# Optimization experiments

Measured on AMD Instinct MI355X. Metric: run time of the kernel, lower is better.

Reference implementation:

```python
import jax, jax.numpy as jnp
import numpy as np

B, S, D, H = 2, 2048, 2048, 16
HD = D // H  # head_dim = 128


def rotate_half(x):
    x1, x2 = x[..., : x.shape[-1] // 2], x[..., x.shape[-1] // 2 :]
    return jnp.concatenate((-x2, x1), axis=-1)


def setup_inputs() -> dict:
    key = jax.random.key(0)
    ks = jax.random.split(key, 6)
    x = jax.random.normal(ks[0], (B, S, D), dtype=jnp.float32)
    # RoPE cos/sin tables, shape [B, S, head_dim]
    inv_freq = 1.0 / (10000.0 ** (np.arange(0, HD, 2, dtype=np.float32) / HD))
    t = np.arange(S, dtype=np.float32)
    freqs = np.outer(t, inv_freq)                      # [S, HD/2]
    emb = np.concatenate([freqs, freqs], axis=-1)      # [S, HD]
    cos = jnp.broadcast_to(jnp.cos(emb), (B, S, HD)).astype(jnp.float32)
    sin = jnp.broadcast_to(jnp.sin(emb), (B, S, HD)).astype(jnp.float32)
    attn_mask = jnp.zeros((B, S), dtype=jnp.float32)   # additive 2D mask
    scale = 0.02
    wq = jax.random.normal(ks[1], (D, D), dtype=jnp.float32) * scale
    wk = jax.random.normal(ks[2], (D, D), dtype=jnp.float32) * scale
    wv = jax.random.normal(ks[3], (D, D), dtype=jnp.float32) * scale
    wo = jax.random.normal(ks[4], (D, D), dtype=jnp.float32) * scale
    return {"x": x, "cos": cos, "sin": sin, "attn_mask": attn_mask,
            "wq": wq, "wk": wk, "wv": wv, "wo": wo}


def reference(x, cos, sin, attn_mask, wq, wk, wv, wo):
    b, s, d = x.shape
    # fused-style QKV projections (nn.Linear: y = x @ W.T), reshape to [b,h,s,hd]
    def proj(w):
        return jnp.einsum('bsd,ed->bse', x, w).reshape(b, s, H, HD).transpose(0, 2, 1, 3)
    q, k, v = proj(wq), proj(wk), proj(wv)
    # RoPE: cos/sin [b,s,hd] -> broadcast over heads
    c = cos[:, None, :, :]
    sn = sin[:, None, :, :]
    q = q * c + rotate_half(q) * sn
    k = k * c + rotate_half(k) * sn
    # SDPA with additive 2D mask -> [b,1,1,s]
    scores = jnp.einsum('bhqd,bhkd->bhqk', q, k) / jnp.sqrt(jnp.float32(HD))
    scores = scores + attn_mask[:, None, None, :]
    attn = jax.nn.softmax(scores, axis=-1)
    out = jnp.einsum('bhqk,bhkd->bhqd', attn, v)
    out = out.transpose(0, 2, 1, 3).reshape(b, s, d)
    return jnp.einsum('bsd,ed->bse', out, wo)
```

## Files before the change

### kernel.cpp

```cpp
#include <hip/hip_runtime.h>

#define B_  2
#define S_  2048
#define D_  2048
#define H_  16
#define HD_ 128

typedef float  f32x4  __attribute__((ext_vector_type(4)));
typedef float  f32x16 __attribute__((ext_vector_type(16)));
typedef __bf16 bf16x8 __attribute__((ext_vector_type(8)));
typedef unsigned int u32;

__device__ __forceinline__ void gl16(const void* g, void* l) {
  __builtin_amdgcn_global_load_lds(
      (const __attribute__((address_space(1))) unsigned int*)g,
      (__attribute__((address_space(3))) unsigned int*)l, 16, 0, 0);
}

__device__ __forceinline__ ushort f2bf(float f) {
  union { float f; unsigned u; } v; v.f = f;
  unsigned r = v.u + 0x7FFFu + ((v.u >> 16) & 1u);
  return (ushort)(r >> 16);
}
__device__ __forceinline__ float bf2f(ushort b) {
  union { unsigned u; float f; } v; v.u = ((unsigned)b) << 16;
  return v.f;
}
__device__ __forceinline__ f32x4 fzero() {
  f32x4 v; v[0] = 0.f; v[1] = 0.f; v[2] = 0.f; v[3] = 0.f; return v;
}
__device__ __forceinline__ float exp2x(float x) {
  return __builtin_amdgcn_exp2f(x);
}

__global__ void cvt_all(const float* __restrict__ x,  const float* __restrict__ wq,
                        const float* __restrict__ wk, const float* __restrict__ wv,
                        const float* __restrict__ wo, ushort* __restrict__ dst)
{
  int i = blockIdx.x * blockDim.x + threadIdx.x;
  if (i >= 6291456) return;
  const float* s;
  int t = i - 2097152;
  if (t < 0)             { s = x;  t = i; }
  else if (t < 1048576)  { s = wq; }
  else if (t < 2097152)  { s = wk; t -= 1048576; }
  else if (t < 3145728)  { s = wv; t -= 2097152; }
  else                   { s = wo; t -= 3145728; }
  float4 v = ((const float4*)s)[t];
  ((ushort4*)dst)[i] = make_ushort4(f2bf(v.x), f2bf(v.y), f2bf(v.z), f2bf(v.w));
}

template<int MODE>
__global__ __launch_bounds__(256, 2)
void gemm_bt(const ushort* __restrict__ A, const ushort* __restrict__ Bp,
             void* __restrict__ Cp, int M, int N, int K)
{
  __shared__ __align__(16) ushort lds[2][2][128 * 32];
  const int tid  = threadIdx.x;
  const int wave = tid >> 6, lane = tid & 63;
  const int qt = lane >> 4, ln = lane & 15;
  const int wr = wave >> 1, wc = wave & 1;
  const int bm = blockIdx.x * 128, bn = blockIdx.y * 128;

  f32x4 acc[4][4];
#pragma unroll
  for (int a = 0; a < 4; ++a)
#pragma unroll
    for (int b = 0; b < 4; ++b) acc[a][b] = fzero();

  auto stage = [&](int buf, int kt) {
#pragma unroll
    for (int it = 0; it < 2; ++it) {
      int c = it * 256 + tid;
      int row = c >> 2, ch = c & 3;
      int chs = ch ^ ((row >> 1) & 3);
      gl16(A  + (size_t)(bm + row) * K + kt + chs * 8,
           (void*)&lds[buf][0][(it * 256 + wave * 64) * 8]);
      gl16(Bp + (size_t)(bn + row) * K + kt + chs * 8,
           (void*)&lds[buf][1][(it * 256 + wave * 64) * 8]);
    }
  };

  const int nk = K >> 5;
  stage(0, 0);
  int cur = 0;
  for (int kt = 0; kt < nk; ++kt) {
    __syncthreads();
    if (kt + 1 < nk) stage(cur ^ 1, (kt + 1) << 5);
    bf16x8 af[4], bfr[4];
#pragma unroll
    for (int mf = 0; mf < 4; ++mf) {
      int row = wr * 64 + mf * 16 + ln;
      int sl = qt ^ ((row >> 1) & 3);
      af[mf] = *(const bf16x8*)&lds[cur][0][row * 32 + sl * 8];
    }
#pragma unroll
    for (int nf = 0; nf < 4; ++nf) {
      int row = wc * 64 + nf * 16 + ln;
      int sl = qt ^ ((row >> 1) & 3);
      bfr[nf] = *(const bf16x8*)&lds[cur][1][row * 32 + sl * 8];
    }
#pragma unroll
    for (int mf = 0; mf < 4; ++mf)
#pragma unroll
      for (int nf = 0; nf < 4; ++nf)
        acc[mf][nf] = __builtin_amdgcn_mfma_f32_16x16x32_bf16(
            af[mf], bfr[nf], acc[mf][nf], 0, 0, 0);
    cur ^= 1;
  }

#pragma unroll
  for (int mf = 0; mf < 4; ++mf)
#pragma unroll
    for (int nf = 0; nf < 4; ++nf) {
      int m0 = bm + wr * 64 + mf * 16 + qt * 4;
      int n  = bn + wc * 64 + nf * 16 + ln;
#pragma unroll
      for (int i = 0; i < 4; ++i) {
        int m = m0 + i;
        if (MODE == 0) {
          ((float*)Cp)[(size_t)m * N + n] = acc[mf][nf][i];
        } else {
          int b = m >> 11, s = m & 2047;
          int h = n >> 7,  d = n & 127;
          if (MODE == 1)
            ((ushort*)Cp)[(((size_t)b * H_ + h) * S_ + s) * HD_ + d] = f2bf(acc[mf][nf][i]);
          else
            ((ushort*)Cp)[(((size_t)b * H_ + h) * HD_ + d) * S_ + s] = f2bf(acc[mf][nf][i]);
        }
      }
    }
}

__global__ void rope_qk(ushort* __restrict__ Q, ushort* __restrict__ Kt,
                        const float* __restrict__ cs, const float* __restrict__ sn)
{
  int t = blockIdx.x * 256 + threadIdx.x;
  int d  = t & 63;
  int rr = t >> 6;
  int isk = rr >> 16;
  int bhs = rr & 65535;
  int s = bhs & 2047;
  int b = bhs >> 15;
  ushort* P = isk ? Kt : Q;
  size_t ro = (size_t)bhs * HD_;
  float q0 = bf2f(P[ro + d]), q1 = bf2f(P[ro + d + 64]);
  size_t ci = ((size_t)b * S_ + s) * HD_ + d;
  float c0 = cs[ci], s0 = sn[ci], c1 = cs[ci + 64], s1 = sn[ci + 64];
  P[ro + d]      = f2bf(q0 * c0 - q1 * s0);
  P[ro + d + 64] = f2bf(q1 * c1 + q0 * s1);
}

__global__ __launch_bounds__(256, 2)
void flash(const ushort* __restrict__ Q, const ushort* __restrict__ Kk,
           const ushort* __restrict__ VT, const float* __restrict__ mask,
           ushort* __restrict__ O)
{
  __shared__ __align__(16) ushort kt_s[2][64 * 128];
  __shared__ __align__(16) ushort vt_s[2][128 * 64];

  const int tid = threadIdx.x;
  const int wave = tid >> 6, lane = tid & 63;
  const int ln32 = lane & 31, hi = lane >> 5;
  const int bh = blockIdx.x, b = bh >> 4, h = bh & 15;
  const size_t base  = (size_t)bh * S_ * HD_;
  const size_t baseT = (size_t)bh * HD_ * S_;
  const int q0 = blockIdx.y * 128 + wave * 32;
  const float L2E = 1.4426950408889634f;
  const float scale2 = 0.08838834764831845f * L2E;

  bf16x8 qf[8];
  {
    const ushort* qrow = Q + base + (size_t)(q0 + ln32) * HD_;
#pragma unroll
    for (int hd = 0; hd < 8; ++hd)
      qf[hd] = *(const bf16x8*)(qrow + hd * 16 + hi * 8);
  }

  f32x16 accO[4];
#pragma unroll
  for (int dblk = 0; dblk < 4; ++dblk)
#pragma unroll
    for (int i = 0; i < 16; ++i) accO[dblk][i] = 0.f;
  float mrun = -1e30f;
  float lrun = 0.f;

  auto stageKV = [&](int buf, int k0) {
#pragma unroll
    for (int it = 0; it < 4; ++it) {
      int c = it * 256 + tid;
      int row = c >> 4, sl = c & 15;
      int chs = (sl - row) & 15;
      gl16(Kk + base + (size_t)(k0 + row) * HD_ + chs * 8,
           (void*)&kt_s[buf][(it * 256 + wave * 64) * 8]);
    }
#pragma unroll
    for (int it = 0; it < 4; ++it) {
      int c = it * 256 + tid;
      int d = c >> 3, sl = c & 7;
      int chs = (sl - d) & 7;
      gl16(VT + baseT + (size_t)d * S_ + k0 + chs * 8,
           (void*)&vt_s[buf][(it * 256 + wave * 64) * 8]);
    }
  };

  stageKV(0, 0);
  int cur = 0;
  for (int k0 = 0; k0 < S_; k0 += 64) {
    __syncthreads();
    if (k0 + 64 < S_) stageKV(cur ^ 1, k0 + 64);

    f32x16 sc[2];
    __builtin_amdgcn_s_setprio(1);
#pragma unroll
    for (int kblk = 0; kblk < 2; ++kblk) {
      f32x16 a;
#pragma unroll
      for (int i = 0; i < 16; ++i) a[i] = 0.f;
      int row = kblk * 32 + ln32;
#pragma unroll
      for (int hd = 0; hd < 8; ++hd) {
        int sl = (hd * 2 + hi + row) & 15;
        bf16x8 kf = *(const bf16x8*)&kt_s[cur][row * 128 + sl * 8];
        a = __builtin_amdgcn_mfma_f32_32x32x16_bf16(kf, qf[hd], a, 0, 0, 0);
      }
      sc[kblk] = a;
    }
    __builtin_amdgcn_s_setprio(0);

    float sv[2][16];
#pragma unroll
    for (int kblk = 0; kblk < 2; ++kblk)
#pragma unroll
      for (int g = 0; g < 4; ++g) {
        float4 mk = *(const float4*)&mask[(size_t)b * S_ + k0 + kblk * 32 + g * 8 + hi * 4];
        sv[kblk][g * 4 + 0] = sc[kblk][g * 4 + 0] * scale2 + mk.x * L2E;
        sv[kblk][g * 4 + 1] = sc[kblk][g * 4 + 1] * scale2 + mk.y * L2E;
        sv[kblk][g * 4 + 2] = sc[kblk][g * 4 + 2] * scale2 + mk.z * L2E;
        sv[kblk][g * 4 + 3] = sc[kblk][g * 4 + 3] * scale2 + mk.w * L2E;
      }

    float m = sv[0][0];
#pragma unroll
    for (int kblk = 0; kblk < 2; ++kblk)
#pragma unroll
      for (int i = 0; i < 16; ++i) m = fmaxf(m, sv[kblk][i]);
    m = fmaxf(m, __shfl_xor(m, 32));

    if (__any(m > mrun + 8.f)) {
      float mn = fmaxf(mrun, m);
      float fsc = exp2x(mrun - mn);
      mrun = mn;
      lrun *= fsc;
      float fq[16];
#pragma unroll
      for (int g = 0; g < 4; ++g)
#pragma unroll
        for (int j = 0; j < 4; ++j)
          fq[g * 4 + j] = __shfl(fsc, j + 8 * g + 4 * hi);
#pragma unroll
      for (int dblk = 0; dblk < 4; ++dblk)
#pragma unroll
        for (int i = 0; i < 16; ++i) accO[dblk][i] *= fq[i];
    }

    float tsum = 0.f;
    ushort pb[2][16];
#pragma unroll
    for (int kblk = 0; kblk < 2; ++kblk)
#pragma unroll
      for (int i = 0; i < 16; ++i) {
        float p = exp2x(sv[kblk][i] - mrun);
        __bf16 pq = (__bf16)p;
        union { __bf16 b; ushort s; } cc; cc.b = pq;
        pb[kblk][i] = cc.s;
        tsum += (float)pq;
      }
    lrun += tsum;

    bf16x8 pa[4];
#pragma unroll
    for (int kblk = 0; kblk < 2; ++kblk) {
      u32 pk0[4], pk1[4];
#pragma unroll
      for (int t = 0; t < 4; ++t) {
        pk0[t] = (u32)pb[kblk][4 * t]     | ((u32)pb[kblk][4 * t + 1] << 16);
        pk1[t] = (u32)pb[kblk][4 * t + 2] | ((u32)pb[kblk][4 * t + 3] << 16);
      }
#pragma unroll
      for (int c = 0; c < 2; ++c) {
        u32 a0 = pk0[2 * c],     a1 = pk1[2 * c];
        u32 b0 = pk0[2 * c + 1], b1 = pk1[2 * c + 1];
        u32 s0 = hi ? a0 : b0,   s1 = hi ? a1 : b1;
        u32 r0 = (u32)__shfl_xor((int)s0, 32);
        u32 r1 = (u32)__shfl_xor((int)s1, 32);
        u32 o0 = hi ? b0 : a0,   o1 = hi ? b1 : a1;
        u32 w[4];
        w[0] = hi ? r0 : o0;  w[1] = hi ? r1 : o1;
        w[2] = hi ? o0 : r0;  w[3] = hi ? o1 : r1;
        pa[kblk * 2 + c] = *(bf16x8*)w;
      }
    }

    __builtin_amdgcn_s_setprio(1);
#pragma unroll
    for (int kk = 0; kk < 4; ++kk)
#pragma unroll
      for (int dblk = 0; dblk < 4; ++dblk) {
        int d = dblk * 32 + ln32;
        int sl = (kk * 2 + hi + d) & 7;
        bf16x8 vf = *(const bf16x8*)&vt_s[cur][d * 64 + sl * 8];
        accO[dblk] = __builtin_amdgcn_mfma_f32_32x32x16_bf16(pa[kk], vf, accO[dblk], 0, 0, 0);
      }
    __builtin_amdgcn_s_setprio(0);
    cur ^= 1;
  }

  lrun += __shfl_xor(lrun, 32);
  float inv_own = 1.f / lrun;
  float invv[16];
#pragma unroll
  for (int g = 0; g < 4; ++g)
#pragma unroll
    for (int j = 0; j < 4; ++j)
      invv[g * 4 + j] = __shfl(inv_own, j + 8 * g + 4 * hi);
#pragma unroll
  for (int dblk = 0; dblk < 4; ++dblk)
#pragma unroll
    for (int g = 0; g < 4; ++g)
#pragma unroll
      for (int j = 0; j < 4; ++j) {
        int q = j + 8 * g + 4 * hi;
        size_t idx = ((size_t)b * S_ + q0 + q) * D_ + h * HD_ + dblk * 32 + ln32;
        O[idx] = f2bf(accO[dblk][g * 4 + j] * invv[g * 4 + j]);
      }
}

extern "C" void kernel_launch(void* const* d_in, const int* in_sizes, int n_in,
                              void* d_out, int out_size, void* d_ws, size_t ws_size,
                              hipStream_t stream)
{
  if (n_in != 8) return;
  if (in_sizes[0] != 8388608) return;
  if (in_sizes[3] != 4096)    return;
  if (out_size != 8388608) return;
  if (ws_size < (size_t)96 * 1024 * 1024) return;

  const float* x    = (const float*)d_in[0];
  const float* cosb = (const float*)d_in[1];
  const float* sinb = (const float*)d_in[2];
  const float* mask = (const float*)d_in[3];
  const float* wq   = (const float*)d_in[4];
  const float* wk   = (const float*)d_in[5];
  const float* wv   = (const float*)d_in[6];
  const float* wo   = (const float*)d_in[7];

  char* ws = (char*)d_ws;
  ushort* xb  = (ushort*)(ws);
  ushort* wqb = (ushort*)(ws + 16777216);
  ushort* wkb = (ushort*)(ws + 25165824);
  ushort* wvb = (ushort*)(ws + 33554432);
  ushort* wob = (ushort*)(ws + 41943040);
  ushort* Qb  = (ushort*)(ws + 50331648);
  ushort* Kb  = (ushort*)(ws + 67108864);
  ushort* VTb = (ushort*)(ws + 83886080);
  ushort* AOb = xb;

  cvt_all<<<24576, 256, 0, stream>>>(x, wq, wk, wv, wo, xb);

  dim3 gg(32, 16);
  gemm_bt<1><<<gg, 256, 0, stream>>>(xb, wqb, Qb,  4096, 2048, 2048);
  gemm_bt<1><<<gg, 256, 0, stream>>>(xb, wkb, Kb,  4096, 2048, 2048);
  gemm_bt<3><<<gg, 256, 0, stream>>>(xb, wvb, VTb, 4096, 2048, 2048);

  rope_qk<<<32768, 256, 0, stream>>>(Qb, Kb, cosb, sinb);

  flash<<<dim3(32, 16), 256, 0, stream>>>(Qb, Kb, VTb, mask, AOb);

  gemm_bt<0><<<gg, 256, 0, stream>>>(AOb, wob, d_out, 4096, 2048, 2048);
}
```

Before: 299.6 us.

## Process two 32-row query blocks per wave in flash attention

Each wave now handles 64 query rows (two 32-row MFMA blocks) instead of 32, so every K and V fragment read from LDS is reused for two MFMAs. The block covers 256 queries, which halves the grid and halves the total K/V staging traffic. Register pressure roughly doubles for accumulators and Q fragments, so launch bounds drop to one block per SM. That cuts occupancy, and the grid of 256 blocks may underfill the 256 CUs.

```diff
diff --git a/kernel.cpp b/kernel.cpp
--- a/kernel.cpp
+++ b/kernel.cpp
@@ -151,7 +151,7 @@
   P[ro + d + 64] = f2bf(q1 * c1 + q0 * s1);
 }
 
-__global__ __launch_bounds__(256, 2)
+__global__ __launch_bounds__(256, 1)
 void flash(const ushort* __restrict__ Q, const ushort* __restrict__ Kk,
            const ushort* __restrict__ VT, const float* __restrict__ mask,
            ushort* __restrict__ O)
@@ -165,25 +165,28 @@
   const int bh = blockIdx.x, b = bh >> 4, h = bh & 15;
   const size_t base  = (size_t)bh * S_ * HD_;
   const size_t baseT = (size_t)bh * HD_ * S_;
-  const int q0 = blockIdx.y * 128 + wave * 32;
+  const int q0 = blockIdx.y * 256 + wave * 64;
   const float L2E = 1.4426950408889634f;
   const float scale2 = 0.08838834764831845f * L2E;
 
-  bf16x8 qf[8];
-  {
-    const ushort* qrow = Q + base + (size_t)(q0 + ln32) * HD_;
+  bf16x8 qf[2][8];
+#pragma unroll
+  for (int qb = 0; qb < 2; ++qb) {
+    const ushort* qrow = Q + base + (size_t)(q0 + qb * 32 + ln32) * HD_;
 #pragma unroll
     for (int hd = 0; hd < 8; ++hd)
-      qf[hd] = *(const bf16x8*)(qrow + hd * 16 + hi * 8);
+      qf[qb][hd] = *(const bf16x8*)(qrow + hd * 16 + hi * 8);
   }
 
-  f32x16 accO[4];
-#pragma unroll
-  for (int dblk = 0; dblk < 4; ++dblk)
-#pragma unroll
-    for (int i = 0; i < 16; ++i) accO[dblk][i] = 0.f;
-  float mrun = -1e30f;
-  float lrun = 0.f;
+  f32x16 accO[2][4];
+#pragma unroll
+  for (int qb = 0; qb < 2; ++qb)
+#pragma unroll
+    for (int dblk = 0; dblk < 4; ++dblk)
+#pragma unroll
+      for (int i = 0; i < 16; ++i) accO[qb][dblk][i] = 0.f;
+  float mrun[2] = {-1e30f, -1e30f};
+  float lrun[2] = {0.f, 0.f};
 
   auto stageKV = [&](int buf, int k0) {
 #pragma unroll
@@ -210,97 +213,113 @@
     __syncthreads();
     if (k0 + 64 < S_) stageKV(cur ^ 1, k0 + 64);
 
-    f32x16 sc[2];
+    f32x16 sc[2][2];
     __builtin_amdgcn_s_setprio(1);
 #pragma unroll
     for (int kblk = 0; kblk < 2; ++kblk) {
-      f32x16 a;
-#pragma unroll
-      for (int i = 0; i < 16; ++i) a[i] = 0.f;
+#pragma unroll
+      for (int i = 0; i < 16; ++i) { sc[0][kblk][i] = 0.f; sc[1][kblk][i] = 0.f; }
       int row = kblk * 32 + ln32;
 #pragma unroll
       for (int hd = 0; hd < 8; ++hd) {
         int sl = (hd * 2 + hi + row) & 15;
         bf16x8 kf = *(const bf16x8*)&kt_s[cur][row * 128 + sl * 8];
-        a = __builtin_amdgcn_mfma_f32_32x32x16_bf16(kf, qf[hd], a, 0, 0, 0);
-      }
-      sc[kblk] = a;
+        sc[0][kblk] = __builtin_amdgcn_mfma_f32_32x32x16_bf16(kf, qf[0][hd], sc[0][kblk], 0, 0, 0);
+        sc[1][kblk] = __builtin_amdgcn_mfma_f32_32x32x16_bf16(kf, qf[1][hd], sc[1][kblk], 0, 0, 0);
+      }
     }
     __builtin_amdgcn_s_setprio(0);
 
-    float sv[2][16];
 #pragma unroll
     for (int kblk = 0; kblk < 2; ++kblk)
 #pragma unroll
       for (int g = 0; g < 4; ++g) {
         float4 mk = *(const float4*)&mask[(size_t)b * S_ + k0 + kblk * 32 + g * 8 + hi * 4];
-        sv[kblk][g * 4 + 0] = sc[kblk][g * 4 + 0] * scale2 + mk.x * L2E;
-        sv[kblk][g * 4 + 1] = sc[kblk][g * 4 + 1] * scale2 + mk.y * L2E;
-        sv[kblk][g * 4 + 2] = sc[kblk][g * 4 + 2] * scale2 + mk.z * L2E;
-        sv[kblk][g * 4 + 3] = sc[kblk][g * 4 + 3] * scale2 + mk.w * L2E;
-      }
-
-    float m = sv[0][0];
-#pragma unroll
-    for (int kblk = 0; kblk < 2; ++kblk)
-#pragma unroll
-      for (int i = 0; i < 16; ++i) m = fmaxf(m, sv[kblk][i]);
-    m = fmaxf(m, __shfl_xor(m, 32));
-
-    if (__any(m > mrun + 8.f)) {
-      float mn = fmaxf(mrun, m);
-      float fsc = exp2x(mrun - mn);
-      mrun = mn;
-      lrun *= fsc;
-      float fq[16];
-#pragma unroll
-      for (int g = 0; g < 4; ++g)
-#pragma unroll
-        for (int j = 0; j < 4; ++j)
-          fq[g * 4 + j] = __shfl(fsc, j + 8 * g + 4 * hi);
-#pragma unroll
-      for (int dblk = 0; dblk < 4; ++dblk)
-#pragma unroll
-        for (int i = 0; i < 16; ++i) accO[dblk][i] *= fq[i];
-    }
-
-    float tsum = 0.f;
-    ushort pb[2][16];
-#pragma unroll
-    for (int kblk = 0; kblk < 2; ++kblk)
-#pragma unroll
-      for (int i = 0; i < 16; ++i) {
-        float p = exp2x(sv[kblk][i] - mrun);
-        __bf16 pq = (__bf16)p;
-        union { __bf16 b; ushort s; } cc; cc.b = pq;
-        pb[kblk][i] = cc.s;
-        tsum += (float)pq;
-      }
-    lrun += tsum;
-
-    bf16x8 pa[4];
-#pragma unroll
-    for (int kblk = 0; kblk < 2; ++kblk) {
-      u32 pk0[4], pk1[4];
-#pragma unroll
-      for (int t = 0; t < 4; ++t) {
-        pk0[t] = (u32)pb[kblk][4 * t]     | ((u32)pb[kblk][4 * t + 1] << 16);
-        pk1[t] = (u32)pb[kblk][4 * t + 2] | ((u32)pb[kblk][4 * t + 3] << 16);
-      }
-#pragma unroll
-      for (int c = 0; c < 2; ++c) {
-        u32 a0 = pk0[2 * c],     a1 = pk1[2 * c];
-        u32 b0 = pk0[2 * c + 1], b1 = pk1[2 * c + 1];
-        u32 s0 = hi ? a0 : b0,   s1 = hi ? a1 : b1;
-        u32 r0 = (u32)__shfl_xor((int)s0, 32);
-        u32 r1 = (u32)__shfl_xor((int)s1, 32);
-        u32 o0 = hi ? b0 : a0,   o1 = hi ? b1 : a1;
-        u32 w[4];
-        w[0] = hi ? r0 : o0;  w[1] = hi ? r1 : o1;
-        w[2] = hi ? o0 : r0;  w[3] = hi ? o1 : r1;
-        pa[kblk * 2 + c] = *(bf16x8*)w;
-      }
-    }
+        float m0 = mk.x * L2E, m1 = mk.y * L2E, m2 = mk.z * L2E, m3 = mk.w * L2E;
+#pragma unroll
+        for (int qb = 0; qb < 2; ++qb) {
+          sc[qb][kblk][g * 4 + 0] = sc[qb][kblk][g * 4 + 0] * scale2 + m0;
+          sc[qb][kblk][g * 4 + 1] = sc[qb][kblk][g * 4 + 1] * scale2 + m1;
+          sc[qb][kblk][g * 4 + 2] = sc[qb][kblk][g * 4 + 2] * scale2 + m2;
+          sc[qb][kblk][g * 4 + 3] = sc[qb][kblk][g * 4 + 3] * scale2 + m3;
+        }
+      }
+
+    float m[2];
+#pragma unroll
+    for (int qb = 0; qb < 2; ++qb) {
+      float mm = sc[qb][0][0];
+#pragma unroll
+      for (int kblk = 0; kblk < 2; ++kblk)
+#pragma unroll
+        for (int i = 0; i < 16; ++i) mm = fmaxf(mm, sc[qb][kblk][i]);
+      mm = fmaxf(mm, __shfl_xor(mm, 32));
+      m[qb] = mm;
+    }
+
+    bool need = (m[0] > mrun[0] + 8.f) | (m[1] > mrun[1] + 8.f);
+    if (__any(need)) {
+#pragma unroll
+      for (int qb = 0; qb < 2; ++qb) {
+        float mn = fmaxf(mrun[qb], m[qb]);
+        float fsc = exp2x(mrun[qb] - mn);
+        mrun[qb] = mn;
+        lrun[qb] *= fsc;
+        float fq[16];
+#pragma unroll
+        for (int g = 0; g < 4; ++g)
+#pragma unroll
+          for (int j = 0; j < 4; ++j)
+            fq[g * 4 + j] = __shfl(fsc, j + 8 * g + 4 * hi);
+#pragma unroll
+        for (int dblk = 0; dblk < 4; ++dblk)
+#pragma unroll
+          for (int i = 0; i < 16; ++i) accO[qb][dblk][i] *= fq[i];
+      }
+    }
+
+    ushort pb[2][2][16];
+#pragma unroll
+    for (int qb = 0; qb < 2; ++qb) {
+      float tsum = 0.f;
+#pragma unroll
+      for (int kblk = 0; kblk < 2; ++kblk)
+#pragma unroll
+        for (int i = 0; i < 16; ++i) {
+          float p = exp2x(sc[qb][kblk][i] - mrun[qb]);
+          __bf16 pq = (__bf16)p;
+          union { __bf16 b; ushort s; } cc; cc.b = pq;
+          pb[qb][kblk][i] = cc.s;
+          tsum += (float)pq;
+        }
+      lrun[qb] += tsum;
+    }
+
+    bf16x8 pa[2][4];
+#pragma unroll
+    for (int qb = 0; qb < 2; ++qb)
+#pragma unroll
+      for (int kblk = 0; kblk < 2; ++kblk) {
+        u32 pk0[4], pk1[4];
+#pragma unroll
+        for (int t = 0; t < 4; ++t) {
+          pk0[t] = (u32)pb[qb][kblk][4 * t]     | ((u32)pb[qb][kblk][4 * t + 1] << 16);
+          pk1[t] = (u32)pb[qb][kblk][4 * t + 2] | ((u32)pb[qb][kblk][4 * t + 3] << 16);
+        }
+#pragma unroll
+        for (int c = 0; c < 2; ++c) {
+          u32 a0 = pk0[2 * c],     a1 = pk1[2 * c];
+          u32 b0 = pk0[2 * c + 1], b1 = pk1[2 * c + 1];
+          u32 s0 = hi ? a0 : b0,   s1 = hi ? a1 : b1;
+          u32 r0 = (u32)__shfl_xor((int)s0, 32);
+          u32 r1 = (u32)__shfl_xor((int)s1, 32);
+          u32 o0 = hi ? b0 : a0,   o1 = hi ? b1 : a1;
+          u32 w[4];
+          w[0] = hi ? r0 : o0;  w[1] = hi ? r1 : o1;
+          w[2] = hi ? o0 : r0;  w[3] = hi ? o1 : r1;
+          pa[qb][kblk * 2 + c] = *(bf16x8*)w;
+        }
+      }
 
     __builtin_amdgcn_s_setprio(1);
 #pragma unroll
@@ -310,30 +329,34 @@
         int d = dblk * 32 + ln32;
         int sl = (kk * 2 + hi + d) & 7;
         bf16x8 vf = *(const bf16x8*)&vt_s[cur][d * 64 + sl * 8];
-        accO[dblk] = __builtin_amdgcn_mfma_f32_32x32x16_bf16(pa[kk], vf, accO[dblk], 0, 0, 0);
+        accO[0][dblk] = __builtin_amdgcn_mfma_f32_32x32x16_bf16(pa[0][kk], vf, accO[0][dblk], 0, 0, 0);
+        accO[1][dblk] = __builtin_amdgcn_mfma_f32_32x32x16_bf16(pa[1][kk], vf, accO[1][dblk], 0, 0, 0);
       }
     __builtin_amdgcn_s_setprio(0);
     cur ^= 1;
   }
 
-  lrun += __shfl_xor(lrun, 32);
-  float inv_own = 1.f / lrun;
-  float invv[16];
-#pragma unroll
-  for (int g = 0; g < 4; ++g)
-#pragma unroll
-    for (int j = 0; j < 4; ++j)
-      invv[g * 4 + j] = __shfl(inv_own, j + 8 * g + 4 * hi);
-#pragma unroll
-  for (int dblk = 0; dblk < 4; ++dblk)
+#pragma unroll
+  for (int qb = 0; qb < 2; ++qb) {
+    float lr = lrun[qb] + __shfl_xor(lrun[qb], 32);
+    float inv_own = 1.f / lr;
+    float invv[16];
 #pragma unroll
     for (int g = 0; g < 4; ++g)
 #pragma unroll
-      for (int j = 0; j < 4; ++j) {
-        int q = j + 8 * g + 4 * hi;
-        size_t idx = ((size_t)b * S_ + q0 + q) * D_ + h * HD_ + dblk * 32 + ln32;
-        O[idx] = f2bf(accO[dblk][g * 4 + j] * invv[g * 4 + j]);
-      }
+      for (int j = 0; j < 4; ++j)
+        invv[g * 4 + j] = __shfl(inv_own, j + 8 * g + 4 * hi);
+#pragma unroll
+    for (int dblk = 0; dblk < 4; ++dblk)
+#pragma unroll
+      for (int g = 0; g < 4; ++g)
+#pragma unroll
+        for (int j = 0; j < 4; ++j) {
+          int q = qb * 32 + j + 8 * g + 4 * hi;
+          size_t idx = ((size_t)b * S_ + q0 + q) * D_ + h * HD_ + dblk * 32 + ln32;
+          O[idx] = f2bf(accO[qb][dblk][g * 4 + j] * invv[g * 4 + j]);
+        }
+  }
 }
 
 extern "C" void kernel_launch(void* const* d_in, const int* in_sizes, int n_in,
@@ -375,7 +398,7 @@
 
   rope_qk<<<32768, 256, 0, stream>>>(Qb, Kb, cosb, sinb);
 
-  flash<<<dim3(32, 16), 256, 0, stream>>>(Qb, Kb, VTb, mask, AOb);
+  flash<<<dim3(32, 8), 256, 0, stream>>>(Qb, Kb, VTb, mask, AOb);
 
   gemm_bt<0><<<gg, 256, 0, stream>>>(AOb, wob, d_out, 4096, 2048, 2048);
 }
```

Result: slower. 342.9 us (+14.4%).
